# Kernel optimization log

Measured on AMD Instinct MI355X. Metric: run time of the kernel, lower is better.

The kernel has to match this reference:

```python
import jax, jax.numpy as jnp
import numpy as np

B, S, D, H, HID = 8192, 16, 128, 8, 1024
DH = D // H  # 16
GCN, NUMF = 40, 103
EPS = 1e-5

def _make_pe():
    pos = np.arange(S, dtype=np.float64)[:, None]
    i = np.arange(D, dtype=np.float64)[None, :]
    pe = pos / np.power(10000.0, (i // 2 * 2.0) / D)
    pe[:, 0::2] = np.sin(pe[:, 0::2])
    pe[:, 1::2] = np.cos(pe[:, 1::2])
    return jnp.asarray(pe, dtype=jnp.float32)  # [S, D]

PE = _make_pe()

def setup_inputs() -> dict:
    key = jax.random.key(0)
    ks = jax.random.split(key, 16)
    rn = lambda k, shape, s=0.02: (jax.random.normal(k, shape, jnp.float32) * s)
    return {
        "x": jax.random.normal(ks[0], (B, S, D), jnp.float32),
        "gcn_i": jax.random.normal(ks[1], (B, GCN), jnp.float32),
        "num": jax.random.normal(ks[2], (B, NUMF), jnp.float32),
        # two independent encoder layers, params stacked on leading dim
        "Wq": rn(ks[3], (2, D, D)), "bq": jnp.zeros((2, D), jnp.float32),
        "Wk": rn(ks[4], (2, D, D)), "bk": jnp.zeros((2, D), jnp.float32),
        "Wv": rn(ks[5], (2, D, D)), "bv": jnp.zeros((2, D), jnp.float32),
        "Wo": rn(ks[6], (2, D, D)), "bo": jnp.zeros((2, D), jnp.float32),
        "ln1_g": jnp.ones((2, D), jnp.float32), "ln1_b": jnp.zeros((2, D), jnp.float32),
        "W1": rn(ks[7], (2, D, HID)), "b1": jnp.zeros((2, HID), jnp.float32),
        "W2": rn(ks[8], (2, HID, D)), "b2": jnp.zeros((2, D), jnp.float32),
        "ln2_g": jnp.ones((2, D), jnp.float32), "ln2_b": jnp.zeros((2, D), jnp.float32),
        # head
        "Wn": rn(ks[9], (NUMF, D)), "bnum": jnp.zeros((D,), jnp.float32),
        "bn_gamma": jnp.ones((D,), jnp.float32), "bn_beta": jnp.zeros((D,), jnp.float32),
        "Wf": rn(ks[10], (S * D + GCN + D, 1)), "bf": jnp.zeros((1,), jnp.float32),
    }

def _ln(x, g, b):
    m = x.mean(-1, keepdims=True)
    v = ((x - m) ** 2).mean(-1, keepdims=True)
    return (x - m) * jax.lax.rsqrt(v + EPS) * g + b

def reference(x, gcn_i, num, Wq, bq, Wk, bk, Wv, bv, Wo, bo, ln1_g, ln1_b,
              W1, b1, W2, b2, ln2_g, ln2_b, Wn, bnum, bn_gamma, bn_beta, Wf, bf):
    out = x + PE  # positional encoding (dropout = identity in eval)
    scale = DH ** -0.5
    for l in range(2):
        # NOTE: original uses a raw .view(B*H, -1, DH) (no transpose) -- faithful reshape
        q = (out @ Wq[l] + bq[l]).reshape(B * H, S, DH)
        k = (out @ Wk[l] + bk[l]).reshape(B * H, S, DH)
        v = (out @ Wv[l] + bv[l]).reshape(B * H, S, DH)
        attn = jax.nn.softmax(jnp.einsum('nsd,ntd->nst', q, k) * scale, axis=-1)
        ctx = jnp.einsum('nst,ntd->nsd', attn, v).reshape(B, S, D)
        h = _ln(ctx @ Wo[l] + bo[l] + out, ln1_g[l], ln1_b[l])
        ff = jax.nn.relu(h @ W1[l] + b1[l]) @ W2[l] + b2[l]
        out = _ln(ff + h, ln2_g[l], ln2_b[l])
    flat = out.reshape(B, S * D)  # [B, 2048]
    n = num @ Wn + bnum  # [B, 128]
    # BatchNorm1d, training-mode forward (biased batch variance)
    mu = n.mean(0)
    var = ((n - mu) ** 2).mean(0)
    n = (n - mu) * jax.lax.rsqrt(var + EPS) * bn_gamma + bn_beta
    p = jnp.concatenate([flat, gcn_i, n], axis=-1)  # [B, 2216]
    return jax.nn.sigmoid(p @ Wf + bf)
```

## Files before the change

kernel.cpp:

```cpp
#include <hip/hip_runtime.h>
#include <hip/hip_bf16.h>
#include <math.h>

#define B_SZ   8192
#define S_SZ   16
#define D_SZ   128
#define HID_SZ 1024
#define NUMF_SZ 103
#define GCN_SZ 40
#define G_B    4
#define NBLK   (B_SZ / G_B)
#define STRD   136

typedef short bh8 __attribute__((ext_vector_type(8)));
typedef float fx4 __attribute__((ext_vector_type(4)));
typedef unsigned short us4 __attribute__((ext_vector_type(4)));

__device__ __forceinline__ fx4 mfma16(bh8 a, bh8 b, fx4 c) {
    return __builtin_amdgcn_mfma_f32_16x16x32_bf16(a, b, c, 0, 0, 0);
}

__device__ __forceinline__ unsigned short f2b(float f) {
    union { __hip_bfloat16 b; unsigned short u; } cv;
    cv.b = __float2bfloat16(f);
    return cv.u;
}
__device__ __forceinline__ float bu2f(unsigned short u) {
    return __uint_as_float(((unsigned)u) << 16);
}

__global__ __launch_bounds__(256) void prep_weights(
    const float* __restrict__ Wq, const float* __restrict__ Wk,
    const float* __restrict__ Wv, const float* __restrict__ Wo,
    const float* __restrict__ W1, const float* __restrict__ W2,
    unsigned short* __restrict__ WswQ, unsigned short* __restrict__ WswK,
    unsigned short* __restrict__ WswV, unsigned short* __restrict__ WswO,
    unsigned short* __restrict__ Wsw1, unsigned short* __restrict__ Wsw2,
    float* __restrict__ PEt)
{
    int i = blockIdx.x * 256 + threadIdx.x;
    if (i < 2048) {
        int s = i >> 7, c = i & 127;
        float expo = (float)((c >> 1) * 2) * (1.0f / 128.0f);
        float denom = powf(10000.0f, expo);
        float ang = (float)s / denom;
        PEt[i] = (c & 1) ? cosf(ang) : sinf(ang);
    }
    if (i < 2 * 16384) {
        int l = i >> 14, r = i & 16383;
        int nt = r >> 11, ks = (r >> 9) & 3, lane = (r >> 3) & 63, e = r & 7;
        int k = ks * 32 + (lane >> 4) * 8 + e;
        int n = nt * 16 + (lane & 15);
        int s = l * 16384 + k * 128 + n;
        WswQ[i] = f2b(Wq[s]); WswK[i] = f2b(Wk[s]);
        WswV[i] = f2b(Wv[s]); WswO[i] = f2b(Wo[s]);
    }
    {
        int l = i >> 17, r = i & 131071;
        int nt = r >> 11, ks = (r >> 9) & 3, lane = (r >> 3) & 63, e = r & 7;
        int k = ks * 32 + (lane >> 4) * 8 + e;
        int n = nt * 16 + (lane & 15);
        Wsw1[i] = f2b(W1[l * 131072 + k * 1024 + n]);
    }
    {
        int l = i >> 17, r = i & 131071;
        int nt = r >> 14, kt = (r >> 9) & 31, lane = (r >> 3) & 63, e = r & 7;
        int k = kt * 32 + (lane >> 4) * 8 + e;
        int n = nt * 16 + (lane & 15);
        Wsw2[i] = f2b(W2[l * 131072 + k * 128 + n]);
    }
}

__global__ __launch_bounds__(256, 2) void encoder_fused(
    const float* __restrict__ x, const float* __restrict__ gcn,
    const float* __restrict__ bq, const float* __restrict__ bk,
    const float* __restrict__ bv, const float* __restrict__ bo,
    const float* __restrict__ ln1g, const float* __restrict__ ln1b,
    const float* __restrict__ b1, const float* __restrict__ b2p,
    const float* __restrict__ ln2g, const float* __restrict__ ln2b,
    const float* __restrict__ Wf,
    const unsigned short* __restrict__ WswQ, const unsigned short* __restrict__ WswK,
    const unsigned short* __restrict__ WswV, const unsigned short* __restrict__ WswO,
    const unsigned short* __restrict__ Wsw1, const unsigned short* __restrict__ Wsw2,
    const float* __restrict__ PEt,
    float* __restrict__ acc1)
{
    __shared__ unsigned short ACT[64][STRD];
    __shared__ unsigned short Qb[64][STRD];
    __shared__ unsigned short Kb[64][STRD];
    __shared__ unsigned short Vb[64][STRD];
    __shared__ float2 LNp2[64][4];
    __shared__ float LNs[64][2];
    __shared__ unsigned short Pb[4][16][16];

    unsigned short* Vb4 = &Vb[0][0];

    const int t = threadIdx.x;
    const int w = t >> 6, lane = t & 63;
    const int q = lane >> 4, ln = lane & 15;
    const int bbase = blockIdx.x * G_B;

    {
        const float4* xb = (const float4*)(x + (size_t)bbase * 2048);
        const float4* pe4 = (const float4*)PEt;
#pragma unroll
        for (int i = 0; i < 8; ++i) {
            int f4 = i * 256 + t;
            float4 xv = xb[f4];
            float4 pv = pe4[f4 & 511];
            int flat = f4 * 4;
            int row = flat >> 7, col = flat & 127;
            ushort4 pk = {f2b(xv.x + pv.x), f2b(xv.y + pv.y),
                          f2b(xv.z + pv.z), f2b(xv.w + pv.w)};
            *(ushort4*)&ACT[row][col] = pk;
        }
    }
    __syncthreads();

    for (int l = 0; l < 2; ++l) {
        {
            bh8 afr[4][4];
#pragma unroll
            for (int mt = 0; mt < 4; ++mt)
#pragma unroll
                for (int ks = 0; ks < 4; ++ks)
                    afr[mt][ks] = *(const bh8*)&ACT[mt * 16 + ln][ks * 32 + q * 8];
#pragma unroll
            for (int mtx = 0; mtx < 2; ++mtx) {
                const unsigned short* Wm = (mtx == 0) ? WswQ + l * 16384 : WswK + l * 16384;
                const float* bias = (mtx == 0) ? bq + l * 128 : bk + l * 128;
                unsigned short (*dst)[STRD] = (mtx == 0) ? Qb : Kb;
#pragma unroll
                for (int i2 = 0; i2 < 2; ++i2) {
                    int nt = w * 2 + i2;
                    bh8 wfr[4];
#pragma unroll
                    for (int ks = 0; ks < 4; ++ks)
                        wfr[ks] = *(const bh8*)(Wm + ((nt * 4 + ks) * 64 + lane) * 8);
                    int n0 = nt * 16 + q * 4;
                    fx4 bb4 = *(const fx4*)&bias[n0];
#pragma unroll
                    for (int mt = 0; mt < 4; ++mt) {
                        fx4 acc = {0.f, 0.f, 0.f, 0.f};
#pragma unroll
                        for (int ks = 0; ks < 4; ++ks) acc = mfma16(wfr[ks], afr[mt][ks], acc);
                        us4 o;
#pragma unroll
                        for (int r2 = 0; r2 < 4; ++r2) o[r2] = f2b(acc[r2] + bb4[r2]);
                        *(us4*)&dst[mt * 16 + ln][n0] = o;
                    }
                }
            }
#pragma unroll
            for (int i2 = 0; i2 < 2; ++i2) {
                int nt = w * 2 + i2;
                bh8 wfr[4];
#pragma unroll
                for (int ks = 0; ks < 4; ++ks)
                    wfr[ks] = *(const bh8*)(WswV + l * 16384 + ((nt * 4 + ks) * 64 + lane) * 8);
                int n = nt * 16 + ln;
                float bb = bv[l * 128 + n];
#pragma unroll
                for (int mt = 0; mt < 4; ++mt) {
                    fx4 acc = {0.f, 0.f, 0.f, 0.f};
#pragma unroll
                    for (int ks = 0; ks < 4; ++ks) acc = mfma16(afr[mt][ks], wfr[ks], acc);
#pragma unroll
                    for (int r2 = 0; r2 < 4; ++r2) {
                        int s = q * 4 + r2;
                        Vb4[(((mt * 8 + (s >> 1)) * 16) + ln) * 16 +
                            (((s & 1) << 3) | nt)] = f2b(acc[r2] + bb);
                    }
                }
            }
        }
        __syncthreads();

        {
            const int E = w;
            const int rbase = E * 16 + (ln >> 3);
            const int ccol = (ln & 7) * 16;
#pragma unroll
            for (int g = 0; g < 8; ++g) {
                bh8 kfr = 0, qfr = 0;
                if (q < 2) {
                    kfr = *(const bh8*)&Kb[rbase + 2 * g][ccol + q * 8];
                    qfr = *(const bh8*)&Qb[rbase + 2 * g][ccol + q * 8];
                }
                fx4 st = mfma16(kfr, qfr, fx4{0.f, 0.f, 0.f, 0.f});
                float p0 = st[0] * 0.25f, p1 = st[1] * 0.25f;
                float p2 = st[2] * 0.25f, p3 = st[3] * 0.25f;
                float mx = fmaxf(fmaxf(p0, p1), fmaxf(p2, p3));
                mx = fmaxf(mx, __shfl_xor(mx, 16));
                mx = fmaxf(mx, __shfl_xor(mx, 32));
                p0 = __expf(p0 - mx); p1 = __expf(p1 - mx);
                p2 = __expf(p2 - mx); p3 = __expf(p3 - mx);
                float sm = (p0 + p1) + (p2 + p3);
                sm += __shfl_xor(sm, 16);
                sm += __shfl_xor(sm, 32);
                float is = 1.0f / sm;
                ushort4 pk = {f2b(p0 * is), f2b(p1 * is), f2b(p2 * is), f2b(p3 * is)};
                *(ushort4*)&Pb[w][ln][q * 4] = pk;
                bh8 vfr = 0, pfr = 0;
                if (q < 2) {
                    vfr = *(const bh8*)&Vb4[(((E * 8 + g) * 16) + ln) * 16 + q * 8];
                    pfr = *(const bh8*)&Pb[w][ln][q * 8];
                }
                fx4 cx = mfma16(vfr, pfr, fx4{0.f, 0.f, 0.f, 0.f});
                ushort4 ck = {f2b(cx[0]), f2b(cx[1]), f2b(cx[2]), f2b(cx[3])};
                *(ushort4*)&Qb[rbase + 2 * g][ccol + q * 4] = ck;
            }
        }
        __syncthreads();

        fx4 Cv[2][4];
        {
            bh8 cfr[4][4];
#pragma unroll
            for (int mt = 0; mt < 4; ++mt)
#pragma unroll
                for (int ks = 0; ks < 4; ++ks)
                    cfr[mt][ks] = *(const bh8*)&Qb[mt * 16 + ln][ks * 32 + q * 8];
#pragma unroll
            for (int i2 = 0; i2 < 2; ++i2) {
                int nt = w * 2 + i2, n0 = nt * 16 + q * 4;
                bh8 wfr[4];
#pragma unroll
                for (int ks = 0; ks < 4; ++ks)
                    wfr[ks] = *(const bh8*)(WswO + l * 16384 + ((nt * 4 + ks) * 64 + lane) * 8);
                fx4 bb4 = *(const fx4*)&bo[l * 128 + n0];
#pragma unroll
                for (int mt = 0; mt < 4; ++mt) {
                    fx4 acc = {0.f, 0.f, 0.f, 0.f};
#pragma unroll
                    for (int ks = 0; ks < 4; ++ks) acc = mfma16(wfr[ks], cfr[mt][ks], acc);
                    us4 rv = *(const us4*)&ACT[mt * 16 + ln][n0];
#pragma unroll
                    for (int r2 = 0; r2 < 4; ++r2)
                        Cv[i2][mt][r2] = acc[r2] + bb4[r2] + bu2f(rv[r2]);
                }
            }
        }
#pragma unroll
        for (int mt = 0; mt < 4; ++mt) {
            float s = 0.f, v = 0.f;
#pragma unroll
            for (int i2 = 0; i2 < 2; ++i2)
#pragma unroll
                for (int r2 = 0; r2 < 4; ++r2) {
                    float a = Cv[i2][mt][r2];
                    s += a; v = fmaf(a, a, v);
                }
            s += __shfl_xor(s, 16); v += __shfl_xor(v, 16);
            s += __shfl_xor(s, 32); v += __shfl_xor(v, 32);
            if (lane < 16) LNp2[mt * 16 + ln][w] = float2{s, v};
        }
        __syncthreads();
        if (t < 64) {
            float2 a0 = LNp2[t][0], a1 = LNp2[t][1];
            float2 a2 = LNp2[t][2], a3 = LNp2[t][3];
            float s = (a0.x + a1.x) + (a2.x + a3.x);
            float v = (a0.y + a1.y) + (a2.y + a3.y);
            float mean = s * (1.0f / 128.0f);
            LNs[t][0] = mean;
            LNs[t][1] = rsqrtf(v * (1.0f / 128.0f) - mean * mean + 1e-5f);
        }
        __syncthreads();
#pragma unroll
        for (int i2 = 0; i2 < 2; ++i2) {
            int n0 = (w * 2 + i2) * 16 + q * 4;
            fx4 gg = *(const fx4*)&ln1g[l * 128 + n0];
            fx4 be = *(const fx4*)&ln1b[l * 128 + n0];
#pragma unroll
            for (int mt = 0; mt < 4; ++mt) {
                int row = mt * 16 + ln;
                float mean = LNs[row][0], inv = LNs[row][1];
                us4 o;
#pragma unroll
                for (int r2 = 0; r2 < 4; ++r2)
                    o[r2] = f2b((Cv[i2][mt][r2] - mean) * inv * gg[r2] + be[r2]);
                *(us4*)&Kb[row][n0] = o;
            }
        }
        __syncthreads();

        bh8 hfr[4][4];
#pragma unroll
        for (int mt = 0; mt < 4; ++mt)
#pragma unroll
            for (int ks = 0; ks < 4; ++ks)
                hfr[mt][ks] = *(const bh8*)&Kb[mt * 16 + ln][ks * 32 + q * 8];
        fx4 f2a[2][4];
#pragma unroll
        for (int i2 = 0; i2 < 2; ++i2)
#pragma unroll
            for (int mt = 0; mt < 4; ++mt) f2a[i2][mt] = fx4{0.f, 0.f, 0.f, 0.f};
        for (int ch = 0; ch < 8; ++ch) {
            unsigned short (*dst)[STRD] = (ch & 1) ? Vb : Qb;
            bh8 w1fr[2][4];
#pragma unroll
            for (int i2 = 0; i2 < 2; ++i2) {
                int ntg = ch * 8 + w * 2 + i2;
#pragma unroll
                for (int ks = 0; ks < 4; ++ks)
                    w1fr[i2][ks] = *(const bh8*)(Wsw1 + l * 131072 + ((ntg * 4 + ks) * 64 + lane) * 8);
            }
#pragma unroll
            for (int mt = 0; mt < 4; ++mt) {
#pragma unroll
                for (int i2 = 0; i2 < 2; ++i2) {
                    fx4 acc = {0.f, 0.f, 0.f, 0.f};
#pragma unroll
                    for (int ks = 0; ks < 4; ++ks) acc = mfma16(w1fr[i2][ks], hfr[mt][ks], acc);
                    int nl0 = (w * 2 + i2) * 16 + q * 4;
                    fx4 bb4 = *(const fx4*)&b1[l * HID_SZ + ch * 128 + nl0];
                    us4 o;
#pragma unroll
                    for (int r2 = 0; r2 < 4; ++r2) {
                        float vv = acc[r2] + bb4[r2];
                        o[r2] = f2b(vv > 0.f ? vv : 0.f);
                    }
                    *(us4*)&dst[mt * 16 + ln][nl0] = o;
                }
            }
            __syncthreads();
            bh8 w2fr[2][4];
#pragma unroll
            for (int i2 = 0; i2 < 2; ++i2)
#pragma unroll
                for (int ks = 0; ks < 4; ++ks)
                    w2fr[i2][ks] = *(const bh8*)(Wsw2 + l * 131072 +
                        (((w * 2 + i2) * 32 + ch * 4 + ks) * 64 + lane) * 8);
#pragma unroll
            for (int mt = 0; mt < 4; ++mt) {
                bh8 ffr[4];
#pragma unroll
                for (int ks = 0; ks < 4; ++ks)
                    ffr[ks] = *(const bh8*)&dst[mt * 16 + ln][ks * 32 + q * 8];
#pragma unroll
                for (int i2 = 0; i2 < 2; ++i2)
#pragma unroll
                    for (int ks = 0; ks < 4; ++ks)
                        f2a[i2][mt] = mfma16(w2fr[i2][ks], ffr[ks], f2a[i2][mt]);
            }
        }
        fx4 Cv2[2][4];
#pragma unroll
        for (int i2 = 0; i2 < 2; ++i2) {
            int n0 = (w * 2 + i2) * 16 + q * 4;
            fx4 bb4 = *(const fx4*)&b2p[l * 128 + n0];
#pragma unroll
            for (int mt = 0; mt < 4; ++mt) {
                us4 rv = *(const us4*)&Kb[mt * 16 + ln][n0];
#pragma unroll
                for (int r2 = 0; r2 < 4; ++r2)
                    Cv2[i2][mt][r2] = f2a[i2][mt][r2] + bb4[r2] + bu2f(rv[r2]);
            }
        }
#pragma unroll
        for (int mt = 0; mt < 4; ++mt) {
            float s = 0.f, v = 0.f;
#pragma unroll
            for (int i2 = 0; i2 < 2; ++i2)
#pragma unroll
                for (int r2 = 0; r2 < 4; ++r2) {
                    float a = Cv2[i2][mt][r2];
                    s += a; v = fmaf(a, a, v);
                }
            s += __shfl_xor(s, 16); v += __shfl_xor(v, 16);
            s += __shfl_xor(s, 32); v += __shfl_xor(v, 32);
            if (lane < 16) LNp2[mt * 16 + ln][w] = float2{s, v};
        }
        __syncthreads();
        if (t < 64) {
            float2 a0 = LNp2[t][0], a1 = LNp2[t][1];
            float2 a2 = LNp2[t][2], a3 = LNp2[t][3];
            float s = (a0.x + a1.x) + (a2.x + a3.x);
            float v = (a0.y + a1.y) + (a2.y + a3.y);
            float mean = s * (1.0f / 128.0f);
            LNs[t][0] = mean;
            LNs[t][1] = rsqrtf(v * (1.0f / 128.0f) - mean * mean + 1e-5f);
        }
        __syncthreads();
#pragma unroll
        for (int i2 = 0; i2 < 2; ++i2) {
            int n0 = (w * 2 + i2) * 16 + q * 4;
            fx4 gg = *(const fx4*)&ln2g[l * 128 + n0];
            fx4 be = *(const fx4*)&ln2b[l * 128 + n0];
#pragma unroll
            for (int mt = 0; mt < 4; ++mt) {
                int row = mt * 16 + ln;
                float mean = LNs[row][0], inv = LNs[row][1];
                us4 o;
#pragma unroll
                for (int r2 = 0; r2 < 4; ++r2)
                    o[r2] = f2b((Cv2[i2][mt][r2] - mean) * inv * gg[r2] + be[r2]);
                *(us4*)&ACT[row][n0] = o;
            }
        }
        __syncthreads();
    }

    {
        int bg = bbase + w;
        float part = 0.f;
        int srow = lane >> 2, c0 = (lane & 3) * 32;
#pragma unroll
        for (int i = 0; i < 4; ++i) {
            bh8 av = *(const bh8*)&ACT[w * 16 + srow][c0 + i * 8];
            int fl = srow * 128 + c0 + i * 8;
#pragma unroll
            for (int e = 0; e < 8; ++e)
                part = fmaf(bu2f((unsigned short)av[e]), Wf[fl + e], part);
        }
        if (lane < GCN_SZ)
            part = fmaf(gcn[(size_t)bg * GCN_SZ + lane], Wf[2048 + lane], part);
#pragma unroll
        for (int off = 32; off; off >>= 1) part += __shfl_xor(part, off);
        if (lane == 0) acc1[bg] = part;
    }
}

__global__ __launch_bounds__(256) void num_stats_kernel(
    const float* __restrict__ num, const float* __restrict__ Wn,
    const float* __restrict__ bnum,
    float* __restrict__ ssum, float* __restrict__ ssq,
    float* __restrict__ nws, int have_nws)
{
    __shared__ float NUM[16][NUMF_SZ + 1];
    __shared__ float cred[4][128];
    const int t = threadIdx.x;
    const int b0 = blockIdx.x * 16;
    const int j = t & 127, sg = t >> 7, s0 = sg * 8;

    for (int idx = t; idx < 16 * NUMF_SZ; idx += 256) {
        int r = idx / NUMF_SZ, f = idx - r * NUMF_SZ;
        NUM[r][f] = num[(size_t)(b0 + r) * NUMF_SZ + f];
    }
    __syncthreads();

    float acc[8];
    float bnv = bnum[j];
#pragma unroll
    for (int r = 0; r < 8; ++r) acc[r] = bnv;
    for (int f = 0; f < NUMF_SZ; ++f) {
        float w = Wn[f * 128 + j];
#pragma unroll
        for (int r = 0; r < 8; ++r) acc[r] = fmaf(NUM[s0 + r][f], w, acc[r]);
    }
    if (have_nws) {
#pragma unroll
        for (int r = 0; r < 8; ++r)
            nws[(size_t)(b0 + s0 + r) * 128 + j] = acc[r];
    }
    float lsum = 0.f, lsq = 0.f;
#pragma unroll
    for (int r = 0; r < 8; ++r) {
        lsum += acc[r];
        lsq = fmaf(acc[r], acc[r], lsq);
    }
    cred[sg][j] = lsum;
    cred[2 + sg][j] = lsq;
    __syncthreads();
    if (sg == 0) atomicAdd(&ssum[j], cred[0][j] + cred[1][j]);
    else         atomicAdd(&ssq[j],  cred[2][j] + cred[3][j]);
}

__global__ __launch_bounds__(128) void bn_coef_kernel(
    const float* __restrict__ ssum, const float* __restrict__ ssq,
    const float* __restrict__ gamma, const float* __restrict__ beta,
    const float* __restrict__ Wf, const float* __restrict__ bfin,
    float* __restrict__ cvec)
{
    const int j = threadIdx.x;
    __shared__ float red2[2];
    float mean = ssum[j] * (1.0f / (float)B_SZ);
    float var = ssq[j] * (1.0f / (float)B_SZ) - mean * mean;
    float inv = rsqrtf(var + 1e-5f);
    float wj = Wf[2088 + j];
    float gi = gamma[j] * inv;
    cvec[j] = gi * wj;
    float k = (beta[j] - mean * gi) * wj;
#pragma unroll
    for (int o = 32; o; o >>= 1) k += __shfl_down(k, o);
    if ((j & 63) == 0) red2[j >> 6] = k;
    __syncthreads();
    if (j == 0) cvec[128] = red2[0] + red2[1] + bfin[0];
}

__global__ __launch_bounds__(256) void final_fast(
    const float* __restrict__ nws, const float* __restrict__ cvec,
    const float* __restrict__ acc1, float* __restrict__ out)
{
    __shared__ float cs[129];
    const int t = threadIdx.x;
    if (t < 129) cs[t] = cvec[t];
    __syncthreads();
    const int w = t >> 6, lane = t & 63;
    const int b = blockIdx.x * 4 + w;
    const float2* nb = (const float2*)(nws + (size_t)b * 128);
    float2 v = nb[lane];
    float d = v.x * cs[2 * lane] + v.y * cs[2 * lane + 1];
#pragma unroll
    for (int o = 32; o; o >>= 1) d += __shfl_xor(d, o);
    if (lane == 0)
        out[b] = 1.0f / (1.0f + __expf(-(acc1[b] + d + cs[128])));
}

__global__ __launch_bounds__(128) void final_kernel(
    const float* __restrict__ num, const float* __restrict__ Wn,
    const float* __restrict__ bnum,
    const float* __restrict__ ssum, const float* __restrict__ ssq,
    const float* __restrict__ gamma, const float* __restrict__ beta,
    const float* __restrict__ Wf, const float* __restrict__ bfin,
    const float* __restrict__ acc1, float* __restrict__ out)
{
    const int b = blockIdx.x, jj = threadIdx.x;
    __shared__ float red2[2];
    __shared__ float NUMr[NUMF_SZ];
    if (jj < NUMF_SZ) NUMr[jj] = num[(size_t)b * NUMF_SZ + jj];
    __syncthreads();
    float nv = bnum[jj];
    for (int f = 0; f < NUMF_SZ; ++f)
        nv = fmaf(NUMr[f], Wn[f * 128 + jj], nv);
    float mean = ssum[jj] * (1.0f / (float)B_SZ);
    float var = ssq[jj] * (1.0f / (float)B_SZ) - mean * mean;
    float bnv = (nv - mean) * rsqrtf(var + 1e-5f) * gamma[jj] + beta[jj];
    float v = bnv * Wf[2088 + jj];
#pragma unroll
    for (int o = 32; o; o >>= 1) v += __shfl_down(v, o);
    if ((jj & 63) == 0) red2[jj >> 6] = v;
    __syncthreads();
    if (jj == 0) {
        float z = acc1[b] + red2[0] + red2[1] + bfin[0];
        out[b] = 1.0f / (1.0f + __expf(-z));
    }
}

extern "C" void kernel_launch(void* const* d_in, const int* in_sizes, int n_in,
                              void* d_out, int out_size, void* d_ws, size_t ws_size,
                              hipStream_t stream)
{
    const float* x    = (const float*)d_in[0];
    const float* gcn  = (const float*)d_in[1];
    const float* num  = (const float*)d_in[2];
    const float* Wq   = (const float*)d_in[3];
    const float* bq   = (const float*)d_in[4];
    const float* Wk   = (const float*)d_in[5];
    const float* bk   = (const float*)d_in[6];
    const float* Wv   = (const float*)d_in[7];
    const float* bv   = (const float*)d_in[8];
    const float* Wo   = (const float*)d_in[9];
    const float* bo   = (const float*)d_in[10];
    const float* ln1g = (const float*)d_in[11];
    const float* ln1b = (const float*)d_in[12];
    const float* W1   = (const float*)d_in[13];
    const float* b1   = (const float*)d_in[14];
    const float* W2   = (const float*)d_in[15];
    const float* b2p  = (const float*)d_in[16];
    const float* ln2g = (const float*)d_in[17];
    const float* ln2b = (const float*)d_in[18];
    const float* Wn   = (const float*)d_in[19];
    const float* bnum = (const float*)d_in[20];
    const float* bng  = (const float*)d_in[21];
    const float* bnb  = (const float*)d_in[22];
    const float* Wf   = (const float*)d_in[23];
    const float* bfin = (const float*)d_in[24];

    float* acc1 = (float*)d_ws;
    float* ssum = acc1 + B_SZ;
    float* ssq  = ssum + 128;
    unsigned short* wb = (unsigned short*)((char*)d_ws + 40960);
    unsigned short* WswQ = wb;
    unsigned short* WswK = wb + 32768;
    unsigned short* WswV = wb + 65536;
    unsigned short* WswO = wb + 98304;
    unsigned short* Wsw1 = wb + 131072;
    unsigned short* Wsw2 = wb + 393216;
    float* PEt = (float*)((char*)d_ws + 40960 + 1310720);
    const size_t nws_off = 40960 + 1310720 + 8192;
    float* nws = (float*)((char*)d_ws + nws_off);
    const size_t cvec_off = nws_off + (size_t)B_SZ * 128 * sizeof(float);
    float* cvec = (float*)((char*)d_ws + cvec_off);
    const int have_nws = (ws_size >= cvec_off + 132 * sizeof(float)) ? 1 : 0;

    hipMemsetAsync(ssum, 0, 2 * 128 * sizeof(float), stream);
    prep_weights<<<1024, 256, 0, stream>>>(Wq, Wk, Wv, Wo, W1, W2,
        WswQ, WswK, WswV, WswO, Wsw1, Wsw2, PEt);
    encoder_fused<<<NBLK, 256, 0, stream>>>(x, gcn, bq, bk, bv, bo,
        ln1g, ln1b, b1, b2p, ln2g, ln2b, Wf,
        WswQ, WswK, WswV, WswO, Wsw1, Wsw2, PEt, acc1);
    num_stats_kernel<<<B_SZ / 16, 256, 0, stream>>>(num, Wn, bnum, ssum, ssq,
        nws, have_nws);
    if (have_nws) {
        bn_coef_kernel<<<1, 128, 0, stream>>>(ssum, ssq, bng, bnb, Wf, bfin, cvec);
        final_fast<<<B_SZ / 4, 256, 0, stream>>>(nws, cvec, acc1, (float*)d_out);
    } else {
        final_kernel<<<B_SZ, 128, 0, stream>>>(num, Wn, bnum, ssum, ssq, bng, bnb,
            Wf, bfin, acc1, (float*)d_out);
    }
}
```

Baseline: 402.8 us.

## Cut encoder LDS with XOR swizzle and buffer reuse; fold BN head into num weights

Drops the padded LDS arrays and the separate V buffer in favour of XOR-swizzled 128-wide tiles. Softmax probabilities are now kept in registers so V can be written into the K buffer, and the scratch space is shared. Together these shrink shared memory enough to raise launch bounds from 2 to 3 blocks per CU. The head no longer stores the [B,128] num projection: the BatchNorm and final-weight coefficients are folded back through Wn into a 103-length vector, so the final kernel reads num directly. The costs are an extra barrier per layer, more register pressure from the preg array and 3-block occupancy, and the loss of the fallback path.

```diff
diff --git a/kernel.cpp b/kernel.cpp
--- a/kernel.cpp
+++ b/kernel.cpp
@@ -10,7 +10,8 @@
 #define GCN_SZ 40
 #define G_B    4
 #define NBLK   (B_SZ / G_B)
-#define STRD   136
+
+#define SW(r, c) (((r) << 7) + ((c) ^ (((r) & 7) << 3)))
 
 typedef short bh8 __attribute__((ext_vector_type(8)));
 typedef float fx4 __attribute__((ext_vector_type(4)));
@@ -27,6 +28,9 @@
 }
 __device__ __forceinline__ float bu2f(unsigned short u) {
     return __uint_as_float(((unsigned)u) << 16);
+}
+__device__ __forceinline__ unsigned int pk2(float a, float b) {
+    return ((unsigned int)f2b(b) << 16) | (unsigned int)f2b(a);
 }
 
 __global__ __launch_bounds__(256) void prep_weights(
@@ -71,7 +75,7 @@
     }
 }
 
-__global__ __launch_bounds__(256, 2) void encoder_fused(
+__global__ __launch_bounds__(256, 3) void encoder_fused(
     const float* __restrict__ x, const float* __restrict__ gcn,
     const float* __restrict__ bq, const float* __restrict__ bk,
     const float* __restrict__ bv, const float* __restrict__ bo,
@@ -85,15 +89,14 @@
     const float* __restrict__ PEt,
     float* __restrict__ acc1)
 {
-    __shared__ unsigned short ACT[64][STRD];
-    __shared__ unsigned short Qb[64][STRD];
-    __shared__ unsigned short Kb[64][STRD];
-    __shared__ unsigned short Vb[64][STRD];
-    __shared__ float2 LNp2[64][4];
-    __shared__ float LNs[64][2];
-    __shared__ unsigned short Pb[4][16][16];
-
-    unsigned short* Vb4 = &Vb[0][0];
+    __shared__ unsigned short ACT[64 * 128];
+    __shared__ unsigned short Qb[64 * 128];
+    __shared__ unsigned short Kb[64 * 128];
+    __shared__ unsigned long long SCRU[384];
+
+    unsigned short* Pb = (unsigned short*)SCRU;
+    float2* LNp2 = (float2*)SCRU;
+    float*  LNs  = (float*)((char*)SCRU + 2048);
 
     const int t = threadIdx.x;
     const int w = t >> 6, lane = t & 63;
@@ -112,103 +115,115 @@
             int row = flat >> 7, col = flat & 127;
             ushort4 pk = {f2b(xv.x + pv.x), f2b(xv.y + pv.y),
                           f2b(xv.z + pv.z), f2b(xv.w + pv.w)};
-            *(ushort4*)&ACT[row][col] = pk;
+            *(ushort4*)&ACT[SW(row, col)] = pk;
         }
     }
     __syncthreads();
 
     for (int l = 0; l < 2; ++l) {
-        {
-            bh8 afr[4][4];
-#pragma unroll
-            for (int mt = 0; mt < 4; ++mt)
-#pragma unroll
-                for (int ks = 0; ks < 4; ++ks)
-                    afr[mt][ks] = *(const bh8*)&ACT[mt * 16 + ln][ks * 32 + q * 8];
-#pragma unroll
-            for (int mtx = 0; mtx < 2; ++mtx) {
-                const unsigned short* Wm = (mtx == 0) ? WswQ + l * 16384 : WswK + l * 16384;
-                const float* bias = (mtx == 0) ? bq + l * 128 : bk + l * 128;
-                unsigned short (*dst)[STRD] = (mtx == 0) ? Qb : Kb;
-#pragma unroll
-                for (int i2 = 0; i2 < 2; ++i2) {
-                    int nt = w * 2 + i2;
-                    bh8 wfr[4];
-#pragma unroll
-                    for (int ks = 0; ks < 4; ++ks)
-                        wfr[ks] = *(const bh8*)(Wm + ((nt * 4 + ks) * 64 + lane) * 8);
-                    int n0 = nt * 16 + q * 4;
-                    fx4 bb4 = *(const fx4*)&bias[n0];
-#pragma unroll
-                    for (int mt = 0; mt < 4; ++mt) {
-                        fx4 acc = {0.f, 0.f, 0.f, 0.f};
-#pragma unroll
-                        for (int ks = 0; ks < 4; ++ks) acc = mfma16(wfr[ks], afr[mt][ks], acc);
-                        us4 o;
-#pragma unroll
-                        for (int r2 = 0; r2 < 4; ++r2) o[r2] = f2b(acc[r2] + bb4[r2]);
-                        *(us4*)&dst[mt * 16 + ln][n0] = o;
-                    }
-                }
-            }
+        bh8 afr[4][4];
+#pragma unroll
+        for (int mt = 0; mt < 4; ++mt)
+#pragma unroll
+            for (int ks = 0; ks < 4; ++ks)
+                afr[mt][ks] = *(const bh8*)&ACT[SW(mt * 16 + ln, ks * 32 + q * 8)];
+
+#pragma unroll
+        for (int mtx = 0; mtx < 2; ++mtx) {
+            const unsigned short* Wm = (mtx == 0) ? WswQ + l * 16384 : WswK + l * 16384;
+            const float* bias = (mtx == 0) ? bq + l * 128 : bk + l * 128;
+            unsigned short* dst = (mtx == 0) ? Qb : Kb;
 #pragma unroll
             for (int i2 = 0; i2 < 2; ++i2) {
                 int nt = w * 2 + i2;
                 bh8 wfr[4];
 #pragma unroll
                 for (int ks = 0; ks < 4; ++ks)
-                    wfr[ks] = *(const bh8*)(WswV + l * 16384 + ((nt * 4 + ks) * 64 + lane) * 8);
-                int n = nt * 16 + ln;
-                float bb = bv[l * 128 + n];
+                    wfr[ks] = *(const bh8*)(Wm + ((nt * 4 + ks) * 64 + lane) * 8);
+                int n0 = nt * 16 + q * 4;
+                fx4 bb4 = *(const fx4*)&bias[n0];
 #pragma unroll
                 for (int mt = 0; mt < 4; ++mt) {
                     fx4 acc = {0.f, 0.f, 0.f, 0.f};
 #pragma unroll
-                    for (int ks = 0; ks < 4; ++ks) acc = mfma16(afr[mt][ks], wfr[ks], acc);
-#pragma unroll
-                    for (int r2 = 0; r2 < 4; ++r2) {
-                        int s = q * 4 + r2;
-                        Vb4[(((mt * 8 + (s >> 1)) * 16) + ln) * 16 +
-                            (((s & 1) << 3) | nt)] = f2b(acc[r2] + bb);
-                    }
+                    for (int ks = 0; ks < 4; ++ks) acc = mfma16(wfr[ks], afr[mt][ks], acc);
+                    us4 o;
+#pragma unroll
+                    for (int r2 = 0; r2 < 4; ++r2) o[r2] = f2b(acc[r2] + bb4[r2]);
+                    *(us4*)&dst[SW(mt * 16 + ln, n0)] = o;
+                }
+            }
+        }
+        __syncthreads();
+
+        const int rbase = w * 16 + (ln >> 3);
+        const int ccol = (ln & 7) * 16;
+        unsigned int preg[8][2];
+#pragma unroll
+        for (int g = 0; g < 8; ++g) {
+            bh8 kfr = 0, qfr = 0;
+            if (q < 2) {
+                kfr = *(const bh8*)&Kb[SW(rbase + 2 * g, ccol + q * 8)];
+                qfr = *(const bh8*)&Qb[SW(rbase + 2 * g, ccol + q * 8)];
+            }
+            fx4 st = mfma16(kfr, qfr, fx4{0.f, 0.f, 0.f, 0.f});
+            float p0 = st[0] * 0.25f, p1 = st[1] * 0.25f;
+            float p2 = st[2] * 0.25f, p3 = st[3] * 0.25f;
+            float mx = fmaxf(fmaxf(p0, p1), fmaxf(p2, p3));
+            mx = fmaxf(mx, __shfl_xor(mx, 16));
+            mx = fmaxf(mx, __shfl_xor(mx, 32));
+            p0 = __expf(p0 - mx); p1 = __expf(p1 - mx);
+            p2 = __expf(p2 - mx); p3 = __expf(p3 - mx);
+            float sm = (p0 + p1) + (p2 + p3);
+            sm += __shfl_xor(sm, 16);
+            sm += __shfl_xor(sm, 32);
+            float is = 1.0f / sm;
+            preg[g][0] = pk2(p0 * is, p1 * is);
+            preg[g][1] = pk2(p2 * is, p3 * is);
+        }
+        __syncthreads();
+
+#pragma unroll
+        for (int i2 = 0; i2 < 2; ++i2) {
+            int nt = w * 2 + i2;
+            bh8 wfr[4];
+#pragma unroll
+            for (int ks = 0; ks < 4; ++ks)
+                wfr[ks] = *(const bh8*)(WswV + l * 16384 + ((nt * 4 + ks) * 64 + lane) * 8);
+            int n = nt * 16 + ln;
+            float bb = bv[l * 128 + n];
+#pragma unroll
+            for (int mt = 0; mt < 4; ++mt) {
+                fx4 acc = {0.f, 0.f, 0.f, 0.f};
+#pragma unroll
+                for (int ks = 0; ks < 4; ++ks) acc = mfma16(afr[mt][ks], wfr[ks], acc);
+#pragma unroll
+                for (int r2 = 0; r2 < 4; ++r2) {
+                    int s = q * 4 + r2;
+                    int flat = (((mt * 8 + (s >> 1)) * 16) + ln) * 16 +
+                               (((s & 1) << 3) | nt);
+                    Kb[SW(flat >> 7, flat & 127)] = f2b(acc[r2] + bb);
                 }
             }
         }
         __syncthreads();
 
         {
-            const int E = w;
-            const int rbase = E * 16 + (ln >> 3);
-            const int ccol = (ln & 7) * 16;
+            unsigned int* Pu = (unsigned int*)Pb;
 #pragma unroll
             for (int g = 0; g < 8; ++g) {
-                bh8 kfr = 0, qfr = 0;
-                if (q < 2) {
-                    kfr = *(const bh8*)&Kb[rbase + 2 * g][ccol + q * 8];
-                    qfr = *(const bh8*)&Qb[rbase + 2 * g][ccol + q * 8];
-                }
-                fx4 st = mfma16(kfr, qfr, fx4{0.f, 0.f, 0.f, 0.f});
-                float p0 = st[0] * 0.25f, p1 = st[1] * 0.25f;
-                float p2 = st[2] * 0.25f, p3 = st[3] * 0.25f;
-                float mx = fmaxf(fmaxf(p0, p1), fmaxf(p2, p3));
-                mx = fmaxf(mx, __shfl_xor(mx, 16));
-                mx = fmaxf(mx, __shfl_xor(mx, 32));
-                p0 = __expf(p0 - mx); p1 = __expf(p1 - mx);
-                p2 = __expf(p2 - mx); p3 = __expf(p3 - mx);
-                float sm = (p0 + p1) + (p2 + p3);
-                sm += __shfl_xor(sm, 16);
-                sm += __shfl_xor(sm, 32);
-                float is = 1.0f / sm;
-                ushort4 pk = {f2b(p0 * is), f2b(p1 * is), f2b(p2 * is), f2b(p3 * is)};
-                *(ushort4*)&Pb[w][ln][q * 4] = pk;
+                int pi = ((w * 16 + ln) * 24 + q * 4) >> 1;
+                Pu[pi] = preg[g][0];
+                Pu[pi + 1] = preg[g][1];
                 bh8 vfr = 0, pfr = 0;
                 if (q < 2) {
-                    vfr = *(const bh8*)&Vb4[(((E * 8 + g) * 16) + ln) * 16 + q * 8];
-                    pfr = *(const bh8*)&Pb[w][ln][q * 8];
+                    int flat = ((w * 8 + g) * 16 + ln) * 16 + q * 8;
+                    vfr = *(const bh8*)&Kb[SW(flat >> 7, flat & 127)];
+                    pfr = *(const bh8*)&Pb[(w * 16 + ln) * 24 + q * 8];
                 }
                 fx4 cx = mfma16(vfr, pfr, fx4{0.f, 0.f, 0.f, 0.f});
                 ushort4 ck = {f2b(cx[0]), f2b(cx[1]), f2b(cx[2]), f2b(cx[3])};
-                *(ushort4*)&Qb[rbase + 2 * g][ccol + q * 4] = ck;
+                *(ushort4*)&Qb[SW(rbase + 2 * g, ccol + q * 4)] = ck;
             }
         }
         __syncthreads();
@@ -220,7 +235,7 @@
             for (int mt = 0; mt < 4; ++mt)
 #pragma unroll
                 for (int ks = 0; ks < 4; ++ks)
-                    cfr[mt][ks] = *(const bh8*)&Qb[mt * 16 + ln][ks * 32 + q * 8];
+                    cfr[mt][ks] = *(const bh8*)&Qb[SW(mt * 16 + ln, ks * 32 + q * 8)];
 #pragma unroll
             for (int i2 = 0; i2 < 2; ++i2) {
                 int nt = w * 2 + i2, n0 = nt * 16 + q * 4;
@@ -234,7 +249,7 @@
                     fx4 acc = {0.f, 0.f, 0.f, 0.f};
 #pragma unroll
                     for (int ks = 0; ks < 4; ++ks) acc = mfma16(wfr[ks], cfr[mt][ks], acc);
-                    us4 rv = *(const us4*)&ACT[mt * 16 + ln][n0];
+                    us4 rv = *(const us4*)&ACT[SW(mt * 16 + ln, n0)];
 #pragma unroll
                     for (int r2 = 0; r2 < 4; ++r2)
                         Cv[i2][mt][r2] = acc[r2] + bb4[r2] + bu2f(rv[r2]);
@@ -253,17 +268,17 @@
                 }
             s += __shfl_xor(s, 16); v += __shfl_xor(v, 16);
             s += __shfl_xor(s, 32); v += __shfl_xor(v, 32);
-            if (lane < 16) LNp2[mt * 16 + ln][w] = float2{s, v};
+            if (lane < 16) LNp2[(mt * 16 + ln) * 4 + w] = float2{s, v};
         }
         __syncthreads();
         if (t < 64) {
-            float2 a0 = LNp2[t][0], a1 = LNp2[t][1];
-            float2 a2 = LNp2[t][2], a3 = LNp2[t][3];
+            float2 a0 = LNp2[t * 4 + 0], a1 = LNp2[t * 4 + 1];
+            float2 a2 = LNp2[t * 4 + 2], a3 = LNp2[t * 4 + 3];
             float s = (a0.x + a1.x) + (a2.x + a3.x);
             float v = (a0.y + a1.y) + (a2.y + a3.y);
             float mean = s * (1.0f / 128.0f);
-            LNs[t][0] = mean;
-            LNs[t][1] = rsqrtf(v * (1.0f / 128.0f) - mean * mean + 1e-5f);
+            LNs[t * 2] = mean;
+            LNs[t * 2 + 1] = rsqrtf(v * (1.0f / 128.0f) - mean * mean + 1e-5f);
         }
         __syncthreads();
 #pragma unroll
@@ -274,12 +289,12 @@
 #pragma unroll
             for (int mt = 0; mt < 4; ++mt) {
                 int row = mt * 16 + ln;
-                float mean = LNs[row][0], inv = LNs[row][1];
+                float mean = LNs[row * 2], inv = LNs[row * 2 + 1];
                 us4 o;
 #pragma unroll
                 for (int r2 = 0; r2 < 4; ++r2)
                     o[r2] = f2b((Cv[i2][mt][r2] - mean) * inv * gg[r2] + be[r2]);
-                *(us4*)&Kb[row][n0] = o;
+                *(us4*)&Kb[SW(row, n0)] = o;
             }
         }
         __syncthreads();
@@ -289,14 +304,14 @@
         for (int mt = 0; mt < 4; ++mt)
 #pragma unroll
             for (int ks = 0; ks < 4; ++ks)
-                hfr[mt][ks] = *(const bh8*)&Kb[mt * 16 + ln][ks * 32 + q * 8];
+                hfr[mt][ks] = *(const bh8*)&Kb[SW(mt * 16 + ln, ks * 32 + q * 8)];
         fx4 f2a[2][4];
 #pragma unroll
         for (int i2 = 0; i2 < 2; ++i2)
 #pragma unroll
             for (int mt = 0; mt < 4; ++mt) f2a[i2][mt] = fx4{0.f, 0.f, 0.f, 0.f};
         for (int ch = 0; ch < 8; ++ch) {
-            unsigned short (*dst)[STRD] = (ch & 1) ? Vb : Qb;
+            unsigned short* dst = (ch & 1) ? ACT : Qb;
             bh8 w1fr[2][4];
 #pragma unroll
             for (int i2 = 0; i2 < 2; ++i2) {
@@ -320,7 +335,7 @@
                         float vv = acc[r2] + bb4[r2];
                         o[r2] = f2b(vv > 0.f ? vv : 0.f);
                     }
-                    *(us4*)&dst[mt * 16 + ln][nl0] = o;
+                    *(us4*)&dst[SW(mt * 16 + ln, nl0)] = o;
                 }
             }
             __syncthreads();
@@ -336,7 +351,7 @@
                 bh8 ffr[4];
 #pragma unroll
                 for (int ks = 0; ks < 4; ++ks)
-                    ffr[ks] = *(const bh8*)&dst[mt * 16 + ln][ks * 32 + q * 8];
+                    ffr[ks] = *(const bh8*)&dst[SW(mt * 16 + ln, ks * 32 + q * 8)];
 #pragma unroll
                 for (int i2 = 0; i2 < 2; ++i2)
 #pragma unroll
@@ -351,7 +366,7 @@
             fx4 bb4 = *(const fx4*)&b2p[l * 128 + n0];
 #pragma unroll
             for (int mt = 0; mt < 4; ++mt) {
-                us4 rv = *(const us4*)&Kb[mt * 16 + ln][n0];
+                us4 rv = *(const us4*)&Kb[SW(mt * 16 + ln, n0)];
 #pragma unroll
                 for (int r2 = 0; r2 < 4; ++r2)
                     Cv2[i2][mt][r2] = f2a[i2][mt][r2] + bb4[r2] + bu2f(rv[r2]);
@@ -369,17 +384,17 @@
                 }
             s += __shfl_xor(s, 16); v += __shfl_xor(v, 16);
             s += __shfl_xor(s, 32); v += __shfl_xor(v, 32);
-            if (lane < 16) LNp2[mt * 16 + ln][w] = float2{s, v};
+            if (lane < 16) LNp2[(mt * 16 + ln) * 4 + w] = float2{s, v};
         }
         __syncthreads();
         if (t < 64) {
-            float2 a0 = LNp2[t][0], a1 = LNp2[t][1];
-            float2 a2 = LNp2[t][2], a3 = LNp2[t][3];
+            float2 a0 = LNp2[t * 4 + 0], a1 = LNp2[t * 4 + 1];
+            float2 a2 = LNp2[t * 4 + 2], a3 = LNp2[t * 4 + 3];
             float s = (a0.x + a1.x) + (a2.x + a3.x);
             float v = (a0.y + a1.y) + (a2.y + a3.y);
             float mean = s * (1.0f / 128.0f);
-            LNs[t][0] = mean;
-            LNs[t][1] = rsqrtf(v * (1.0f / 128.0f) - mean * mean + 1e-5f);
+            LNs[t * 2] = mean;
+            LNs[t * 2 + 1] = rsqrtf(v * (1.0f / 128.0f) - mean * mean + 1e-5f);
         }
         __syncthreads();
 #pragma unroll
@@ -390,12 +405,12 @@
 #pragma unroll
             for (int mt = 0; mt < 4; ++mt) {
                 int row = mt * 16 + ln;
-                float mean = LNs[row][0], inv = LNs[row][1];
+                float mean = LNs[row * 2], inv = LNs[row * 2 + 1];
                 us4 o;
 #pragma unroll
                 for (int r2 = 0; r2 < 4; ++r2)
                     o[r2] = f2b((Cv2[i2][mt][r2] - mean) * inv * gg[r2] + be[r2]);
-                *(us4*)&ACT[row][n0] = o;
+                *(us4*)&ACT[SW(row, n0)] = o;
             }
         }
         __syncthreads();
@@ -407,7 +422,7 @@
         int srow = lane >> 2, c0 = (lane & 3) * 32;
 #pragma unroll
         for (int i = 0; i < 4; ++i) {
-            bh8 av = *(const bh8*)&ACT[w * 16 + srow][c0 + i * 8];
+            bh8 av = *(const bh8*)&ACT[SW(w * 16 + srow, c0 + i * 8)];
             int fl = srow * 128 + c0 + i * 8;
 #pragma unroll
             for (int e = 0; e < 8; ++e)
@@ -424,8 +439,7 @@
 __global__ __launch_bounds__(256) void num_stats_kernel(
     const float* __restrict__ num, const float* __restrict__ Wn,
     const float* __restrict__ bnum,
-    float* __restrict__ ssum, float* __restrict__ ssq,
-    float* __restrict__ nws, int have_nws)
+    float* __restrict__ ssum, float* __restrict__ ssq)
 {
     __shared__ float NUM[16][NUMF_SZ + 1];
     __shared__ float cred[4][128];
@@ -448,11 +462,6 @@
 #pragma unroll
         for (int r = 0; r < 8; ++r) acc[r] = fmaf(NUM[s0 + r][f], w, acc[r]);
     }
-    if (have_nws) {
-#pragma unroll
-        for (int r = 0; r < 8; ++r)
-            nws[(size_t)(b0 + s0 + r) * 128 + j] = acc[r];
-    }
     float lsum = 0.f, lsq = 0.f;
 #pragma unroll
     for (int r = 0; r < 8; ++r) {
@@ -470,71 +479,50 @@
     const float* __restrict__ ssum, const float* __restrict__ ssq,
     const float* __restrict__ gamma, const float* __restrict__ beta,
     const float* __restrict__ Wf, const float* __restrict__ bfin,
+    const float* __restrict__ Wn, const float* __restrict__ bnum,
     float* __restrict__ cvec)
 {
     const int j = threadIdx.x;
+    __shared__ float cS[128];
     __shared__ float red2[2];
     float mean = ssum[j] * (1.0f / (float)B_SZ);
     float var = ssq[j] * (1.0f / (float)B_SZ) - mean * mean;
     float inv = rsqrtf(var + 1e-5f);
     float wj = Wf[2088 + j];
     float gi = gamma[j] * inv;
-    cvec[j] = gi * wj;
-    float k = (beta[j] - mean * gi) * wj;
+    float cj = gi * wj;
+    cS[j] = cj;
+    float k = (beta[j] - mean * gi) * wj + bnum[j] * cj;
 #pragma unroll
     for (int o = 32; o; o >>= 1) k += __shfl_down(k, o);
     if ((j & 63) == 0) red2[j >> 6] = k;
     __syncthreads();
-    if (j == 0) cvec[128] = red2[0] + red2[1] + bfin[0];
+    if (j == 0) cvec[103] = red2[0] + red2[1] + bfin[0];
+    if (j < NUMF_SZ) {
+        float s = 0.f;
+        for (int jj = 0; jj < 128; ++jj)
+            s = fmaf(Wn[j * 128 + jj], cS[jj], s);
+        cvec[j] = s;
+    }
 }
 
 __global__ __launch_bounds__(256) void final_fast(
-    const float* __restrict__ nws, const float* __restrict__ cvec,
+    const float* __restrict__ num, const float* __restrict__ cvec,
     const float* __restrict__ acc1, float* __restrict__ out)
 {
-    __shared__ float cs[129];
+    __shared__ float wv[104];
     const int t = threadIdx.x;
-    if (t < 129) cs[t] = cvec[t];
+    if (t < 104) wv[t] = cvec[t];
     __syncthreads();
     const int w = t >> 6, lane = t & 63;
     const int b = blockIdx.x * 4 + w;
-    const float2* nb = (const float2*)(nws + (size_t)b * 128);
-    float2 v = nb[lane];
-    float d = v.x * cs[2 * lane] + v.y * cs[2 * lane + 1];
-#pragma unroll
-    for (int o = 32; o; o >>= 1) d += __shfl_xor(d, o);
+    const float* nb = num + (size_t)b * NUMF_SZ;
+    float part = nb[lane] * wv[lane];
+    if (lane < NUMF_SZ - 64) part += nb[64 + lane] * wv[64 + lane];
+#pragma unroll
+    for (int o = 32; o; o >>= 1) part += __shfl_xor(part, o);
     if (lane == 0)
-        out[b] = 1.0f / (1.0f + __expf(-(acc1[b] + d + cs[128])));
-}
-
-__global__ __launch_bounds__(128) void final_kernel(
-    const float* __restrict__ num, const float* __restrict__ Wn,
-    const float* __restrict__ bnum,
-    const float* __restrict__ ssum, const float* __restrict__ ssq,
-    const float* __restrict__ gamma, const float* __restrict__ beta,
-    const float* __restrict__ Wf, const float* __restrict__ bfin,
-    const float* __restrict__ acc1, float* __restrict__ out)
-{
-    const int b = blockIdx.x, jj = threadIdx.x;
-    __shared__ float red2[2];
-    __shared__ float NUMr[NUMF_SZ];
-    if (jj < NUMF_SZ) NUMr[jj] = num[(size_t)b * NUMF_SZ + jj];
-    __syncthreads();
-    float nv = bnum[jj];
-    for (int f = 0; f < NUMF_SZ; ++f)
-        nv = fmaf(NUMr[f], Wn[f * 128 + jj], nv);
-    float mean = ssum[jj] * (1.0f / (float)B_SZ);
-    float var = ssq[jj] * (1.0f / (float)B_SZ) - mean * mean;
-    float bnv = (nv - mean) * rsqrtf(var + 1e-5f) * gamma[jj] + beta[jj];
-    float v = bnv * Wf[2088 + jj];
-#pragma unroll
-    for (int o = 32; o; o >>= 1) v += __shfl_down(v, o);
-    if ((jj & 63) == 0) red2[jj >> 6] = v;
-    __syncthreads();
-    if (jj == 0) {
-        float z = acc1[b] + red2[0] + red2[1] + bfin[0];
-        out[b] = 1.0f / (1.0f + __expf(-z));
-    }
+        out[b] = 1.0f / (1.0f + __expf(-(acc1[b] + part + wv[103])));
 }
 
 extern "C" void kernel_launch(void* const* d_in, const int* in_sizes, int n_in,
@@ -578,11 +566,7 @@
     unsigned short* Wsw1 = wb + 131072;
     unsigned short* Wsw2 = wb + 393216;
     float* PEt = (float*)((char*)d_ws + 40960 + 1310720);
-    const size_t nws_off = 40960 + 1310720 + 8192;
-    float* nws = (float*)((char*)d_ws + nws_off);
-    const size_t cvec_off = nws_off + (size_t)B_SZ * 128 * sizeof(float);
-    float* cvec = (float*)((char*)d_ws + cvec_off);
-    const int have_nws = (ws_size >= cvec_off + 132 * sizeof(float)) ? 1 : 0;
+    float* cvec = (float*)((char*)d_ws + 40960 + 1310720 + 8192);
 
     hipMemsetAsync(ssum, 0, 2 * 128 * sizeof(float), stream);
     prep_weights<<<1024, 256, 0, stream>>>(Wq, Wk, Wv, Wo, W1, W2,
@@ -590,13 +574,8 @@
     encoder_fused<<<NBLK, 256, 0, stream>>>(x, gcn, bq, bk, bv, bo,
         ln1g, ln1b, b1, b2p, ln2g, ln2b, Wf,
         WswQ, WswK, WswV, WswO, Wsw1, Wsw2, PEt, acc1);
-    num_stats_kernel<<<B_SZ / 16, 256, 0, stream>>>(num, Wn, bnum, ssum, ssq,
-        nws, have_nws);
-    if (have_nws) {
-        bn_coef_kernel<<<1, 128, 0, stream>>>(ssum, ssq, bng, bnb, Wf, bfin, cvec);
-        final_fast<<<B_SZ / 4, 256, 0, stream>>>(nws, cvec, acc1, (float*)d_out);
-    } else {
-        final_kernel<<<B_SZ, 128, 0, stream>>>(num, Wn, bnum, ssum, ssq, bng, bnb,
-            Wf, bfin, acc1, (float*)d_out);
-    }
-}
+    num_stats_kernel<<<B_SZ / 16, 256, 0, stream>>>(num, Wn, bnum, ssum, ssq);
+    bn_coef_kernel<<<1, 128, 0, stream>>>(ssum, ssq, bng, bnb, Wf, bfin,
+        Wn, bnum, cvec);
+    final_fast<<<B_SZ / 4, 256, 0, stream>>>(num, cvec, acc1, (float*)d_out);
+}
```

New measurement: 588.6 us. +46.1%, slower.
